# Kernel optimization log

Measured on AMD Instinct MI355X. Metric: run time of the kernel, lower is better.

The kernel has to match this reference:

```python
import jax, jax.numpy as jnp
import numpy as np

N = 500_000      # total nodes across all graphs in batch
B = 128          # batch_size (number of graphs)
S = 128          # state_size
D = 128          # aggregated_size


def setup_inputs() -> dict:
    key = jax.random.key(0)
    k1, k2, k3, k4, k5, k6 = jax.random.split(key, 6)
    nodes = jax.random.normal(k1, (N, S), dtype=jnp.float32)
    owner_masks = jax.random.randint(k2, (B, N), 0, 2, dtype=jnp.int32)
    # Linear params (torch Linear: y = x @ W.T + b); store W as [in, out] for x @ W
    scale = 1.0 / np.sqrt(S)
    Wt = jax.random.uniform(k3, (S, D), jnp.float32, -scale, scale)
    bt = jax.random.uniform(k4, (D,), jnp.float32, -scale, scale)
    Wg = jax.random.uniform(k5, (S, D), jnp.float32, -scale, scale)
    bg = jax.random.uniform(k6, (D,), jnp.float32, -scale, scale)
    return {"nodes": nodes, "owner_masks": owner_masks,
            "Wt": Wt, "bt": bt, "Wg": Wg, "bg": bg}


def reference(nodes, owner_masks, Wt, bt, Wg, bg):
    # gates = sigmoid(nodes @ Wg + bg)   [N, D]
    gates = jax.nn.sigmoid(nodes @ Wg + bg)
    # data = nodes @ Wt + bt             [N, D]
    data = nodes @ Wt + bt
    # pooled = owner_masks.float() @ (data * gates)   [B, D]
    return owner_masks.astype(jnp.float32) @ (data * gates)
```

## Files before the change

### kernel.cpp

```cpp
#include <hip/hip_runtime.h>


#define NTOT   500000
#define NBLK   512
#define NCHUNK 15625

typedef unsigned long long u64;
typedef unsigned int u32;

typedef __attribute__((ext_vector_type(8))) unsigned short ushort8;
typedef __bf16 bf16x8 __attribute__((ext_vector_type(8)));
typedef __attribute__((ext_vector_type(4))) float f32x4;

static __device__ __forceinline__ u32 f2bf1(float f) {
  u32 u = __float_as_uint(f);
  u += 0x7fffu + ((u >> 16) & 1u);
  return u >> 16;
}

static __device__ __forceinline__ u32 f2bf2(float a, float b) {
  return f2bf1(a) | (f2bf1(b) << 16);
}

static __device__ __forceinline__ u32 bits2bf2(u32 byte, int j) {
  return ((byte >> j) & 1u ? 0x3F80u : 0u) | ((byte >> (j + 1)) & 1u ? 0x3F800000u : 0u);
}

template <bool ATOMIC>
__global__ __launch_bounds__(512, 4)
void agg_main(const float* __restrict__ nodes, const int* __restrict__ masks,
              const float* __restrict__ Wt, const float* __restrict__ bt,
              const float* __restrict__ Wg, const float* __restrict__ bg,
              float* __restrict__ outp) {
  __shared__ __align__(16) unsigned short nodes_s[32][136];
  __shared__ __align__(16) u64 bits[128][17];
  __shared__ __align__(16) unsigned short vt_s[128][40];

  const int tid = threadIdx.x;
  const int lane = tid & 63;
  const int w = tid >> 6;
  const int q = lane >> 4;
  const int r = lane & 15;

  const int bid = blockIdx.x;
  const int c0 = (int)(((long long)bid * NCHUNK) >> 9);
  const int c1 = (int)(((long long)(bid + 1) * NCHUNK) >> 9);
  const int nch = c1 - c0;
  const int n0 = c0 * 32;

  {
    const int row0 = w * 16;
    int cb = 16 * lane;
    if (cb >= nch * 32) cb = 0;
    int4 cur[4], nxt[4];
    auto ldrow = [&](int rr, int4* dst) {
      const int* p = masks + (size_t)(row0 + rr) * NTOT + n0 + cb;
#pragma unroll
      for (int i = 0; i < 4; ++i) dst[i] = *(const int4*)(p + 4 * i);
    };
    ldrow(0, cur);
#pragma unroll 4
    for (int rr = 0; rr < 16; ++rr) {
      if (rr < 15) ldrow(rr + 1, nxt);
      const int* m = (const int*)cur;
      u32 b = 0;
#pragma unroll
      for (int e = 0; e < 16; ++e) b |= (u32)(m[e] != 0) << e;
      ((unsigned short*)bits)[(row0 + rr) * 68 + lane] = (unsigned short)b;
#pragma unroll
      for (int i = 0; i < 4; ++i) cur[i] = nxt[i];
    }
  }

  bf16x8 Wf[2][4];
  float btr, bgr;
  {
    const int d = w * 16 + r;
    btr = bt[d];
    bgr = bg[d];
#pragma unroll
    for (int ks = 0; ks < 4; ++ks) {
      u32 wv[4], gv[4];
#pragma unroll
      for (int j = 0; j < 4; ++j) {
        const int k = ks * 32 + q * 8 + 2 * j;
        wv[j] = f2bf2(Wt[k * 128 + d], Wt[(k + 1) * 128 + d]);
        gv[j] = f2bf2(Wg[k * 128 + d], Wg[(k + 1) * 128 + d]);
      }
      Wf[0][ks] = __builtin_bit_cast(bf16x8, *(ushort8*)wv);
      Wf[1][ks] = __builtin_bit_cast(bf16x8, *(ushort8*)gv);
    }
  }

  const f32x4 fzero = {0.f, 0.f, 0.f, 0.f};
  f32x4 acc[8];
#pragma unroll
  for (int i = 0; i < 8; ++i) acc[i] = fzero;

  float4 nf[2];
  auto issue = [&](int cloc) {
    const int k0 = n0 + cloc * 32;
#pragma unroll
    for (int it = 0; it < 2; ++it) {
      const int flat = it * 512 + tid;
      const int nrow = flat >> 5, nc4 = flat & 31;
      nf[it] = *(const float4*)(nodes + (size_t)(k0 + nrow) * 128 + nc4 * 4);
    }
  };

  issue(0);
  __syncthreads();

  const u32* bitw = (const u32*)bits;

  for (int c = 0; c < nch; ++c) {
    if (c) __syncthreads();
#pragma unroll
    for (int it = 0; it < 2; ++it) {
      const int flat = it * 512 + tid;
      const int nrow = flat >> 5, nc4 = flat & 31;
      const u32 lo = f2bf2(nf[it].x, nf[it].y);
      const u32 hi = f2bf2(nf[it].z, nf[it].w);
      *(u64*)&nodes_s[nrow][nc4 * 4] = (u64)lo | ((u64)hi << 32);
    }
    __syncthreads();
    if (c + 1 < nch) issue(c + 1);

    f32x4 aD[2], aG[2];
    aD[0] = fzero; aD[1] = fzero; aG[0] = fzero; aG[1] = fzero;
#pragma unroll
    for (int ks = 0; ks < 4; ++ks) {
      bf16x8 a0 = *(const bf16x8*)&nodes_s[r][ks * 32 + q * 8];
      bf16x8 a1 = *(const bf16x8*)&nodes_s[16 + r][ks * 32 + q * 8];
      aD[0] = __builtin_amdgcn_mfma_f32_16x16x32_bf16(a0, Wf[0][ks], aD[0], 0, 0, 0);
      aD[1] = __builtin_amdgcn_mfma_f32_16x16x32_bf16(a1, Wf[0][ks], aD[1], 0, 0, 0);
      aG[0] = __builtin_amdgcn_mfma_f32_16x16x32_bf16(a0, Wf[1][ks], aG[0], 0, 0, 0);
      aG[1] = __builtin_amdgcn_mfma_f32_16x16x32_bf16(a1, Wf[1][ks], aG[1], 0, 0, 0);
    }

    const int d = w * 16 + r;
#pragma unroll
    for (int mt = 0; mt < 2; ++mt) {
      float v[4];
#pragma unroll
      for (int reg = 0; reg < 4; ++reg) {
        const float x = aD[mt][reg] + btr;
        const float g = aG[mt][reg] + bgr;
        v[reg] = x * __builtin_amdgcn_rcpf(1.f + __expf(-g));
      }
      const u32 lo = f2bf2(v[0], v[1]);
      const u32 hi = f2bf2(v[2], v[3]);
      *(u64*)&vt_s[d][mt * 16 + q * 4] = (u64)lo | ((u64)hi << 32);
    }

    bf16x8 bfr = *(const bf16x8*)&vt_s[d][q * 8];
#pragma unroll
    for (int mt = 0; mt < 8; ++mt) {
      const u32 dw = bitw[(mt * 16 + r) * 34 + c];
      const u32 byte = (dw >> (q * 8)) & 0xffu;
      u32 p[4];
      p[0] = bits2bf2(byte, 0);
      p[1] = bits2bf2(byte, 2);
      p[2] = bits2bf2(byte, 4);
      p[3] = bits2bf2(byte, 6);
      bf16x8 a = __builtin_bit_cast(bf16x8, *(ushort8*)p);
      acc[mt] = __builtin_amdgcn_mfma_f32_16x16x32_bf16(a, bfr, acc[mt], 0, 0, 0);
    }
  }

#pragma unroll
  for (int mt = 0; mt < 8; ++mt)
#pragma unroll
    for (int reg = 0; reg < 4; ++reg) {
      const int b = mt * 16 + q * 4 + reg;
      const int d = w * 16 + r;
      if (ATOMIC)
        atomicAdd(&outp[b * 128 + d], acc[mt][reg]);
      else
        outp[(size_t)bid * 16384 + b * 128 + d] = acc[mt][reg];
    }
}

__global__ __launch_bounds__(256)
void agg_reduce(const float* __restrict__ part, float* __restrict__ out) {
  const int gid = blockIdx.x * 256 + threadIdx.x;
  const int i = gid & 16383;
  const int grp = gid >> 14;
  const float* p = part + (size_t)grp * 64 * 16384 + i;
  float s = 0.f;
#pragma unroll 8
  for (int g = 0; g < 64; ++g) s += p[(size_t)g * 16384];
  atomicAdd(&out[i], s);
}

extern "C" void kernel_launch(void* const* d_in, const int* in_sizes, int n_in,
                              void* d_out, int out_size, void* d_ws, size_t ws_size,
                              hipStream_t stream) {
  const float* nodes = (const float*)d_in[0];
  const int*   masks = (const int*)d_in[1];
  const float* Wt    = (const float*)d_in[2];
  const float* bt    = (const float*)d_in[3];
  const float* Wg    = (const float*)d_in[4];
  const float* bg    = (const float*)d_in[5];
  float* out = (float*)d_out;

  (void)hipMemsetAsync(d_out, 0, (size_t)out_size * sizeof(float), stream);

  const size_t need = (size_t)NBLK * 16384 * sizeof(float);
  if (ws_size >= need) {
    agg_main<false><<<NBLK, 512, 0, stream>>>(nodes, masks, Wt, bt, Wg, bg, (float*)d_ws);
    agg_reduce<<<512, 256, 0, stream>>>((const float*)d_ws, out);
  } else {
    agg_main<true><<<NBLK, 512, 0, stream>>>(nodes, masks, Wt, bt, Wg, bg, out);
  }
}
```

Baseline: 535.6 us.

## Split fused kernel into gated-projection and mask-pooling kernels via bf16 workspace

Separates the computation into one kernel that computes gated data = (nodes@Wt+bt)*sigmoid(nodes@Wg+bg) and writes it as bf16 tiles to workspace, and a second kernel that builds mask bitsets and does the pooling MFMA from those tiles. The projection kernel uses 1024 blocks and a double-buffered LDS stage so the next chunk's loads overlap compute. The pool kernel splits warps across batch and feature tiles. This removes the serialised per-chunk dependence and syncs of the fused design, at the cost of writing and re-reading an extra 128 MB intermediate.

```diff
diff --git a/kernel.cpp b/kernel.cpp
--- a/kernel.cpp
+++ b/kernel.cpp
@@ -2,8 +2,9 @@
 
 
 #define NTOT   500000
-#define NBLK   512
 #define NCHUNK 15625
+#define NBLK1  1024
+#define NBLK2  512
 
 typedef unsigned long long u64;
 typedef unsigned int u32;
@@ -17,21 +18,228 @@
   u += 0x7fffu + ((u >> 16) & 1u);
   return u >> 16;
 }
-
 static __device__ __forceinline__ u32 f2bf2(float a, float b) {
   return f2bf1(a) | (f2bf1(b) << 16);
 }
-
 static __device__ __forceinline__ u32 bits2bf2(u32 byte, int j) {
   return ((byte >> j) & 1u ? 0x3F80u : 0u) | ((byte >> (j + 1)) & 1u ? 0x3F800000u : 0u);
 }
 
+__global__ __launch_bounds__(512, 4)
+void agg_v(const float* __restrict__ nodes,
+           const float* __restrict__ Wt, const float* __restrict__ bt,
+           const float* __restrict__ Wg, const float* __restrict__ bg,
+           unsigned short* __restrict__ vt) {
+  __shared__ __align__(16) unsigned short nodes_s[2][32][136];
+
+  const int tid = threadIdx.x;
+  const int lane = tid & 63;
+  const int w = tid >> 6;
+  const int q = lane >> 4;
+  const int r = lane & 15;
+
+  const int bid = blockIdx.x;
+  const int c0 = (int)(((long long)bid * NCHUNK) >> 10);
+  const int c1 = (int)(((long long)(bid + 1) * NCHUNK) >> 10);
+  const int nch = c1 - c0;
+  const int n0 = c0 * 32;
+
+  bf16x8 Wf[2][4];
+  float btr, bgr;
+  {
+    const int d = w * 16 + r;
+    btr = bt[d];
+    bgr = bg[d];
+#pragma unroll
+    for (int ks = 0; ks < 4; ++ks) {
+      u32 wv[4], gv[4];
+#pragma unroll
+      for (int j = 0; j < 4; ++j) {
+        const int k = ks * 32 + q * 8 + 2 * j;
+        wv[j] = f2bf2(Wt[k * 128 + d], Wt[(k + 1) * 128 + d]);
+        gv[j] = f2bf2(Wg[k * 128 + d], Wg[(k + 1) * 128 + d]);
+      }
+      Wf[0][ks] = __builtin_bit_cast(bf16x8, *(ushort8*)wv);
+      Wf[1][ks] = __builtin_bit_cast(bf16x8, *(ushort8*)gv);
+    }
+  }
+
+  float4 nf[2];
+  auto issue = [&](int cloc) {
+    const int k0 = n0 + cloc * 32;
+#pragma unroll
+    for (int it = 0; it < 2; ++it) {
+      const int flat = it * 512 + tid;
+      const int nrow = flat >> 5, nc4 = flat & 31;
+      nf[it] = *(const float4*)(nodes + (size_t)(k0 + nrow) * 128 + nc4 * 4);
+    }
+  };
+  auto stage = [&](int buf) {
+#pragma unroll
+    for (int it = 0; it < 2; ++it) {
+      const int flat = it * 512 + tid;
+      const int nrow = flat >> 5, nc4 = flat & 31;
+      const u32 lo = f2bf2(nf[it].x, nf[it].y);
+      const u32 hi = f2bf2(nf[it].z, nf[it].w);
+      *(u64*)&nodes_s[buf][nrow][nc4 * 4] = (u64)lo | ((u64)hi << 32);
+    }
+  };
+
+  issue(0);
+  stage(0);
+
+  const f32x4 fzero = {0.f, 0.f, 0.f, 0.f};
+  const int d = w * 16 + r;
+
+  for (int c = 0; c < nch; ++c) {
+    __syncthreads();
+    if (c + 1 < nch) issue(c + 1);
+    const int buf = c & 1;
+
+    f32x4 aD[2], aG[2];
+    aD[0] = fzero; aD[1] = fzero; aG[0] = fzero; aG[1] = fzero;
+#pragma unroll
+    for (int ks = 0; ks < 4; ++ks) {
+      bf16x8 a0 = *(const bf16x8*)&nodes_s[buf][r][ks * 32 + q * 8];
+      bf16x8 a1 = *(const bf16x8*)&nodes_s[buf][16 + r][ks * 32 + q * 8];
+      aD[0] = __builtin_amdgcn_mfma_f32_16x16x32_bf16(a0, Wf[0][ks], aD[0], 0, 0, 0);
+      aD[1] = __builtin_amdgcn_mfma_f32_16x16x32_bf16(a1, Wf[0][ks], aD[1], 0, 0, 0);
+      aG[0] = __builtin_amdgcn_mfma_f32_16x16x32_bf16(a0, Wf[1][ks], aG[0], 0, 0, 0);
+      aG[1] = __builtin_amdgcn_mfma_f32_16x16x32_bf16(a1, Wf[1][ks], aG[1], 0, 0, 0);
+    }
+
+    unsigned short* base = vt + (size_t)(c0 + c) * 4096 + d * 32;
+#pragma unroll
+    for (int mt = 0; mt < 2; ++mt) {
+      float v[4];
+#pragma unroll
+      for (int reg = 0; reg < 4; ++reg) {
+        const float x = aD[mt][reg] + btr;
+        const float g = aG[mt][reg] + bgr;
+        v[reg] = x * __builtin_amdgcn_rcpf(1.f + __expf(-g));
+      }
+      const u32 lo = f2bf2(v[0], v[1]);
+      const u32 hi = f2bf2(v[2], v[3]);
+      *(u64*)(base + mt * 16 + q * 4) = (u64)lo | ((u64)hi << 32);
+    }
+
+    if (c + 1 < nch) stage((c + 1) & 1);
+  }
+}
+
 template <bool ATOMIC>
 __global__ __launch_bounds__(512, 4)
-void agg_main(const float* __restrict__ nodes, const int* __restrict__ masks,
-              const float* __restrict__ Wt, const float* __restrict__ bt,
-              const float* __restrict__ Wg, const float* __restrict__ bg,
+void agg_pool(const int* __restrict__ masks, const unsigned short* __restrict__ vt,
               float* __restrict__ outp) {
+  __shared__ __align__(16) u64 bits[128][17];
+
+  const int tid = threadIdx.x;
+  const int lane = tid & 63;
+  const int w = tid >> 6;
+  const int q = lane >> 4;
+  const int r = lane & 15;
+
+  const int bid = blockIdx.x;
+  const int c0 = (int)(((long long)bid * NCHUNK) >> 9);
+  const int c1 = (int)(((long long)(bid + 1) * NCHUNK) >> 9);
+  const int nch = c1 - c0;
+  const int n0 = c0 * 32;
+
+  {
+    const int row0 = w * 16;
+    int cb = 16 * lane;
+    if (cb >= nch * 32) cb = 0;
+    int4 cur[4], nxt[4];
+    auto ldrow = [&](int rr, int4* dst) {
+      const int* p = masks + (size_t)(row0 + rr) * NTOT + n0 + cb;
+#pragma unroll
+      for (int i = 0; i < 4; ++i) dst[i] = *(const int4*)(p + 4 * i);
+    };
+    ldrow(0, cur);
+#pragma unroll 4
+    for (int rr = 0; rr < 16; ++rr) {
+      if (rr < 15) ldrow(rr + 1, nxt);
+      const int* m = (const int*)cur;
+      u32 b = 0;
+#pragma unroll
+      for (int e = 0; e < 16; ++e) b |= (u32)(m[e] != 0) << e;
+      ((unsigned short*)bits)[(row0 + rr) * 68 + lane] = (unsigned short)b;
+#pragma unroll
+      for (int i = 0; i < 4; ++i) cur[i] = nxt[i];
+    }
+  }
+  __syncthreads();
+
+  const int wd = w >> 1, wb = w & 1;
+  const int d0 = wd * 32, b0 = wb * 64;
+
+  const f32x4 fzero = {0.f, 0.f, 0.f, 0.f};
+  f32x4 acc[4][2];
+#pragma unroll
+  for (int i = 0; i < 4; ++i) { acc[i][0] = fzero; acc[i][1] = fzero; }
+
+  const u32* bitw = (const u32*)bits;
+
+  bf16x8 vb[2], vbn[2];
+  auto loadv = [&](int cloc, bf16x8* dst) {
+    const unsigned short* base = vt + (size_t)(c0 + cloc) * 4096 + q * 8;
+#pragma unroll
+    for (int nt = 0; nt < 2; ++nt)
+      dst[nt] = *(const bf16x8*)(base + (d0 + nt * 16 + r) * 32);
+  };
+
+  loadv(0, vb);
+  for (int c = 0; c < nch; ++c) {
+    if (c + 1 < nch) loadv(c + 1, vbn);
+#pragma unroll
+    for (int mt = 0; mt < 4; ++mt) {
+      const u32 dw = bitw[(b0 + mt * 16 + r) * 34 + c];
+      const u32 byte = (dw >> (q * 8)) & 0xffu;
+      u32 p[4];
+      p[0] = bits2bf2(byte, 0);
+      p[1] = bits2bf2(byte, 2);
+      p[2] = bits2bf2(byte, 4);
+      p[3] = bits2bf2(byte, 6);
+      bf16x8 a = __builtin_bit_cast(bf16x8, *(ushort8*)p);
+      acc[mt][0] = __builtin_amdgcn_mfma_f32_16x16x32_bf16(a, vb[0], acc[mt][0], 0, 0, 0);
+      acc[mt][1] = __builtin_amdgcn_mfma_f32_16x16x32_bf16(a, vb[1], acc[mt][1], 0, 0, 0);
+    }
+    vb[0] = vbn[0];
+    vb[1] = vbn[1];
+  }
+
+#pragma unroll
+  for (int mt = 0; mt < 4; ++mt)
+#pragma unroll
+    for (int nt = 0; nt < 2; ++nt)
+#pragma unroll
+      for (int reg = 0; reg < 4; ++reg) {
+        const int b = b0 + mt * 16 + q * 4 + reg;
+        const int d = d0 + nt * 16 + r;
+        if (ATOMIC)
+          atomicAdd(&outp[b * 128 + d], acc[mt][nt][reg]);
+        else
+          outp[(size_t)bid * 16384 + b * 128 + d] = acc[mt][nt][reg];
+      }
+}
+
+__global__ __launch_bounds__(256)
+void agg_reduce(const float* __restrict__ part, float* __restrict__ out) {
+  const int gid = blockIdx.x * 256 + threadIdx.x;
+  const int i = gid & 16383;
+  const int grp = gid >> 14;
+  const float* p = part + (size_t)grp * 64 * 16384 + i;
+  float s = 0.f;
+#pragma unroll 8
+  for (int g = 0; g < 64; ++g) s += p[(size_t)g * 16384];
+  atomicAdd(&out[i], s);
+}
+
+__global__ __launch_bounds__(512, 4)
+void agg_fused(const float* __restrict__ nodes, const int* __restrict__ masks,
+               const float* __restrict__ Wt, const float* __restrict__ bt,
+               const float* __restrict__ Wg, const float* __restrict__ bg,
+               float* __restrict__ outp) {
   __shared__ __align__(16) unsigned short nodes_s[32][136];
   __shared__ __align__(16) u64 bits[128][17];
   __shared__ __align__(16) unsigned short vt_s[128][40];
@@ -174,23 +382,8 @@
     for (int reg = 0; reg < 4; ++reg) {
       const int b = mt * 16 + q * 4 + reg;
       const int d = w * 16 + r;
-      if (ATOMIC)
-        atomicAdd(&outp[b * 128 + d], acc[mt][reg]);
-      else
-        outp[(size_t)bid * 16384 + b * 128 + d] = acc[mt][reg];
-    }
-}
-
-__global__ __launch_bounds__(256)
-void agg_reduce(const float* __restrict__ part, float* __restrict__ out) {
-  const int gid = blockIdx.x * 256 + threadIdx.x;
-  const int i = gid & 16383;
-  const int grp = gid >> 14;
-  const float* p = part + (size_t)grp * 64 * 16384 + i;
-  float s = 0.f;
-#pragma unroll 8
-  for (int g = 0; g < 64; ++g) s += p[(size_t)g * 16384];
-  atomicAdd(&out[i], s);
+      atomicAdd(&outp[b * 128 + d], acc[mt][reg]);
+    }
 }
 
 extern "C" void kernel_launch(void* const* d_in, const int* in_sizes, int n_in,
@@ -206,11 +399,20 @@
 
   (void)hipMemsetAsync(d_out, 0, (size_t)out_size * sizeof(float), stream);
 
-  const size_t need = (size_t)NBLK * 16384 * sizeof(float);
-  if (ws_size >= need) {
-    agg_main<false><<<NBLK, 512, 0, stream>>>(nodes, masks, Wt, bt, Wg, bg, (float*)d_ws);
-    agg_reduce<<<512, 256, 0, stream>>>((const float*)d_ws, out);
+  const size_t vt_bytes = (size_t)NCHUNK * 4096 * sizeof(unsigned short);
+  const size_t part_bytes = (size_t)NBLK2 * 16384 * sizeof(float);
+
+  if (ws_size >= vt_bytes + part_bytes) {
+    unsigned short* vt = (unsigned short*)d_ws;
+    float* part = (float*)((char*)d_ws + vt_bytes);
+    agg_v<<<NBLK1, 512, 0, stream>>>(nodes, Wt, bt, Wg, bg, vt);
+    agg_pool<false><<<NBLK2, 512, 0, stream>>>(masks, vt, part);
+    agg_reduce<<<512, 256, 0, stream>>>(part, out);
+  } else if (ws_size >= vt_bytes) {
+    unsigned short* vt = (unsigned short*)d_ws;
+    agg_v<<<NBLK1, 512, 0, stream>>>(nodes, Wt, bt, Wg, bg, vt);
+    agg_pool<true><<<NBLK2, 512, 0, stream>>>(masks, vt, out);
   } else {
-    agg_main<true><<<NBLK, 512, 0, stream>>>(nodes, masks, Wt, bt, Wg, bg, out);
-  }
-}
+    agg_fused<<<512, 512, 0, stream>>>(nodes, masks, Wt, bt, Wg, bg, out);
+  }
+}
```

Result: slower. 569.9 us (+6.4%).
